# Performance work log

Hardware: AMD Instinct MI355X
Metric: run time of the kernel (lower is better)

Reference implementation:

```python
import jax, jax.numpy as jnp
import numpy as np

N = 50000       # nodes
E = 800000      # edges (avg degree 16)
H2, H1, D_IN = 64, 128, 256
BN_EPS = 1e-5


def setup_inputs() -> dict:
    key = jax.random.key(0)
    ks = jax.random.split(key, 8)
    return {
        "y_features": jax.random.normal(ks[0], (N, H2), dtype=jnp.float32),
        "edge_src": jax.random.randint(ks[1], (E,), 0, N, dtype=jnp.int32),
        "edge_dst": jax.random.randint(ks[2], (E,), 0, N, dtype=jnp.int32),
        "edge_weight": jax.random.uniform(ks[3], (E,), dtype=jnp.float32),
        "W1": jax.random.normal(ks[4], (H2, H1), dtype=jnp.float32) * (1.0 / np.sqrt(H2)),
        "gamma1": jnp.ones((H1,), jnp.float32),
        "beta1": jnp.zeros((H1,), jnp.float32),
        "W2": jax.random.normal(ks[5], (H1, D_IN), dtype=jnp.float32) * (1.0 / np.sqrt(H1)),
        "gamma2": jnp.ones((D_IN,), jnp.float32),
        "beta2": jnp.zeros((D_IN,), jnp.float32),
    }


def _gcn_layer(x, W, src, dst, w):
    # dropout(p=0) -> support = x @ W -> spmm(adj, support) -> ReLU
    support = x @ W                                   # [N, Dout]
    msgs = support[src] * w[:, None]                  # [E, Dout]
    agg = jax.ops.segment_sum(msgs, dst, num_segments=N)
    return jax.nn.relu(agg)


def _batchnorm(h, gamma, beta):
    # BatchNorm1d in training mode: batch stats over nodes, biased variance
    mean = jnp.mean(h, axis=0)
    var = jnp.var(h, axis=0)
    return gamma * (h - mean) * jax.lax.rsqrt(var + BN_EPS) + beta


def reference(y_features, edge_src, edge_dst, edge_weight,
              W1, gamma1, beta1, W2, gamma2, beta2):
    h1 = _gcn_layer(y_features, W1, edge_src, edge_dst, edge_weight)
    h1 = _batchnorm(h1, gamma1, beta1)
    h2 = _gcn_layer(h1, W2, edge_src, edge_dst, edge_weight)
    h2 = _batchnorm(h2, gamma2, beta2)
    return h2
```

## Files before the change

### kernel.cpp

```cpp
#include <hip/hip_runtime.h>

#define NN 50000
#define NE 800000

typedef unsigned short ushort_t;
typedef __attribute__((ext_vector_type(8))) short short8;
typedef __attribute__((ext_vector_type(4))) float f32x4;

constexpr int NB   = (NN + 127) / 128;
constexpr int BCAP = 4096;
constexpr int CH     = 1024;
constexpr int NBLK_E = (NE + CH - 1) / CH;
constexpr int NBLK_M = (NN + 63) / 64;
constexpr int NY4    = NN * 64 / 4;
constexpr int CVT_N  = NY4 + 128 * 64 + 256 * 128 + 768;

__device__ __forceinline__ float bf2f(ushort_t u) {
    union { unsigned int i; float f; } v;
    v.i = ((unsigned int)u) << 16;
    return v.f;
}
__device__ __forceinline__ float bf2f_u(unsigned int lo16) {
    union { unsigned int i; float f; } v;
    v.i = lo16 << 16;
    return v.f;
}
__device__ __forceinline__ float hi16_as_f(unsigned int u) {
    union { unsigned int i; float f; } v;
    v.i = u & 0xffff0000u;
    return v.f;
}
__device__ __forceinline__ ushort_t f2bf(float f) {
    union { float f; unsigned int u; } v;
    v.f = f;
    unsigned int r = (v.u + 0x7fffu + ((v.u >> 16) & 1u)) >> 16;
    return (ushort_t)r;
}


__global__ void cvt_all_k(const float* __restrict__ y, const float* __restrict__ W1,
                          const float* __restrict__ W2, ushort_t* __restrict__ ybf,
                          ushort_t* __restrict__ w1t, ushort_t* __restrict__ w2t,
                          float* __restrict__ stats) {
    int i = blockIdx.x * blockDim.x + threadIdx.x;
    if (i < NY4) {
        float4 v = reinterpret_cast<const float4*>(y)[i];
        ushort4 o;
        o.x = f2bf(v.x); o.y = f2bf(v.y); o.z = f2bf(v.z); o.w = f2bf(v.w);
        reinterpret_cast<ushort4*>(ybf)[i] = o;
    } else if (i < NY4 + 128 * 64) {
        int j = i - NY4;
        int c = j >> 6, k = j & 63;
        w1t[j] = f2bf(W1[k * 128 + c]);
    } else if (i < NY4 + 128 * 64 + 256 * 128) {
        int j = i - NY4 - 128 * 64;
        int c = j >> 7, k = j & 127;
        w2t[j] = f2bf(W2[k * 256 + c]);
    } else if (i < CVT_N) {
        stats[i - (NY4 + 128 * 64 + 256 * 128)] = 0.f;
    }
}


__global__ void bblk_k(const int* __restrict__ src, const int* __restrict__ dst,
                       const float* __restrict__ w, uint2* __restrict__ tmp,
                       int* __restrict__ cnt, int E) {
    __shared__ int lcnt[NB], lcur[NB];
    __shared__ int sm[256];
    __shared__ uint2 rec[CH];
    int b = blockIdx.x, tid = threadIdx.x;
    int e0 = b * CH;
    int ec = min(CH, E - e0);
    for (int i = tid; i < NB; i += 256) lcnt[i] = 0;
    __syncthreads();
    for (int i = tid; i < ec; i += 256)
        atomicAdd(&lcnt[dst[e0 + i] >> 7], 1);
    __syncthreads();
    {
        int i0 = tid * 2;
        int v0 = (i0 < NB) ? lcnt[i0] : 0;
        int v1 = (i0 + 1 < NB) ? lcnt[i0 + 1] : 0;
        int s = v0 + v1;
        sm[tid] = s;
        __syncthreads();
        for (int off = 1; off < 256; off <<= 1) {
            int x = (tid >= off) ? sm[tid - off] : 0;
            __syncthreads();
            sm[tid] += x;
            __syncthreads();
        }
        int excl = sm[tid] - s;
        if (i0 < NB) lcur[i0] = excl;
        if (i0 + 1 < NB) lcur[i0 + 1] = excl + v0;
    }
    __syncthreads();
    for (int q = tid; q < NB; q += 256)
        cnt[q * NBLK_E + b] = (lcnt[q] << 16) | lcur[q];
    __syncthreads();
    for (int i = tid; i < ec; i += 256) {
        int d = dst[e0 + i];
        int p = atomicAdd(&lcur[d >> 7], 1);
        uint2 r;
        r.x = (unsigned int)src[e0 + i] | ((unsigned int)(d & 127) << 16);
        r.y = ((unsigned int)f2bf(w[e0 + i])) << 16;
        rec[p] = r;
    }
    __syncthreads();
    for (int i = tid; i < ec; i += 256)
        tmp[(size_t)e0 + i] = rec[i];
}

__global__ void bstat_k(const int* __restrict__ cnt, int* __restrict__ btot) {
    __shared__ int red[256];
    int q = blockIdx.x, tid = threadIdx.x;
    int s = 0;
    for (int b = tid; b < NBLK_E; b += 256) s += cnt[q * NBLK_E + b] >> 16;
    red[tid] = s;
    __syncthreads();
    for (int off = 128; off > 0; off >>= 1) {
        if (tid < off) red[tid] += red[tid + off];
        __syncthreads();
    }
    if (tid == 0) btot[q] = red[0];
}

__global__ void bsort_k(const uint2* __restrict__ tmp, const int* __restrict__ cnt,
                        const int* __restrict__ btot, int* __restrict__ rp,
                        unsigned int* __restrict__ epack, int n) {
    __shared__ int rstart[NBLK_E + 1], rlofs[NBLK_E], rcnt[NBLK_E];
    __shared__ int c128[128], cur128[128], ex128[128];
    __shared__ int pre[256];
    __shared__ int s_start;
    __shared__ uint2 rec8[BCAP];
    __shared__ unsigned int spk[BCAP];
    int q = blockIdx.x, tid = threadIdx.x;
    int d0 = q * 128;
    for (int b = tid; b < NBLK_E; b += 256) {
        int v = cnt[q * NBLK_E + b];
        rcnt[b]  = v >> 16;
        rlofs[b] = v & 0xffff;
    }
    if (tid < 128) c128[tid] = 0;
    {
        int part = 0;
        for (int b = tid; b < q; b += 256) part += btot[b];
        pre[tid] = part;
        __syncthreads();
        for (int off = 128; off > 0; off >>= 1) {
            if (tid < off) pre[tid] += pre[tid + off];
            __syncthreads();
        }
        if (tid == 0) {
            s_start = pre[0];
            if (q == 0) rp[n] = NE;
        }
        __syncthreads();
    }
    int start = s_start;
    {
        int b0 = tid * 4;
        int w0 = (b0 + 0 < NBLK_E) ? rcnt[b0 + 0] : 0;
        int w1 = (b0 + 1 < NBLK_E) ? rcnt[b0 + 1] : 0;
        int w2 = (b0 + 2 < NBLK_E) ? rcnt[b0 + 2] : 0;
        int w3 = (b0 + 3 < NBLK_E) ? rcnt[b0 + 3] : 0;
        int s = w0 + w1 + w2 + w3;
        pre[tid] = s;
        __syncthreads();
        for (int off = 1; off < 256; off <<= 1) {
            int x = (tid >= off) ? pre[tid - off] : 0;
            __syncthreads();
            pre[tid] += x;
            __syncthreads();
        }
        int excl = pre[tid] - s;
        if (b0 + 0 < NBLK_E) rstart[b0 + 0] = excl;
        if (b0 + 1 < NBLK_E) rstart[b0 + 1] = excl + w0;
        if (b0 + 2 < NBLK_E) rstart[b0 + 2] = excl + w0 + w1;
        if (b0 + 3 < NBLK_E) rstart[b0 + 3] = excl + w0 + w1 + w2;
        if (tid == 255) rstart[NBLK_E] = pre[255];
    }
    __syncthreads();
    int total = min(rstart[NBLK_E], BCAP);
    for (int i = tid; i < total; i += 256) {
        int lo = 0, hi = NBLK_E;
        while (hi - lo > 1) {
            int mid = (lo + hi) >> 1;
            if (rstart[mid] <= i) lo = mid; else hi = mid;
        }
        uint2 r = tmp[(size_t)lo * CH + rlofs[lo] + (i - rstart[lo])];
        rec8[i] = r;
        atomicAdd(&c128[(r.x >> 16) & 127], 1);
    }
    __syncthreads();
    if (tid == 0) {
        int run = 0;
        for (int d = 0; d < 128; ++d) { ex128[d] = run; cur128[d] = run; run += c128[d]; }
    }
    __syncthreads();
    if (tid < 128 && d0 + tid < n) rp[d0 + tid] = start + ex128[tid];
    for (int i = tid; i < total; i += 256) {
        uint2 r = rec8[i];
        int p = atomicAdd(&cur128[(r.x >> 16) & 127], 1);
        spk[p] = r.y | (r.x & 0xffffu);
    }
    __syncthreads();
    for (int i = tid; i < total; i += 256)
        epack[start + i] = spk[i];
}


__global__ void spmm1_k(const ushort_t* __restrict__ yb, const int* __restrict__ rp,
                        const unsigned int* __restrict__ ep,
                        ushort_t* __restrict__ t1, int n) {
    int wid  = (blockIdx.x * blockDim.x + threadIdx.x) >> 6;
    int lane = threadIdx.x & 63;
    if (wid >= n) return;
    int beg = rp[wid], end = rp[wid + 1];
    float acc = 0.f;
    int p = beg;
    for (; p + 16 <= end; p += 16) {
        unsigned int m[16];
#pragma unroll
        for (int j = 0; j < 16; ++j) m[j] = ep[p + j];
        ushort_t u[16];
#pragma unroll
        for (int j = 0; j < 16; ++j)
            u[j] = yb[(size_t)(m[j] & 0xffffu) * 64 + lane];
#pragma unroll
        for (int j = 0; j < 16; ++j)
            acc = fmaf(hi16_as_f(m[j]), bf2f(u[j]), acc);
    }
    for (; p + 4 <= end; p += 4) {
        unsigned int m[4];
#pragma unroll
        for (int j = 0; j < 4; ++j) m[j] = ep[p + j];
        ushort_t u[4];
#pragma unroll
        for (int j = 0; j < 4; ++j)
            u[j] = yb[(size_t)(m[j] & 0xffffu) * 64 + lane];
#pragma unroll
        for (int j = 0; j < 4; ++j)
            acc = fmaf(hi16_as_f(m[j]), bf2f(u[j]), acc);
    }
    for (; p < end; ++p) {
        unsigned int m = ep[p];
        acc = fmaf(hi16_as_f(m), bf2f(yb[(size_t)(m & 0xffffu) * 64 + lane]), acc);
    }
    t1[(size_t)wid * 64 + lane] = f2bf(acc);
}

__global__ void spmm2_k(const ushort_t* __restrict__ h1, const int* __restrict__ rp,
                        const unsigned int* __restrict__ ep,
                        const float* __restrict__ colsum1, const float* __restrict__ colsq1,
                        const float* __restrict__ gamma1, const float* __restrict__ beta1,
                        ushort_t* __restrict__ a2, int n) {
    int wid  = (blockIdx.x * blockDim.x + threadIdx.x) >> 6;
    int lane = threadIdx.x & 63;
    if (wid >= n) return;
    int beg = rp[wid], end = rp[wid + 1];
    float a0 = 0.f, a1 = 0.f, wacc = 0.f;
    int p = beg;
    for (; p + 16 <= end; p += 16) {
        unsigned int m[16];
#pragma unroll
        for (int j = 0; j < 16; ++j) m[j] = ep[p + j];
        unsigned int u[16];
#pragma unroll
        for (int j = 0; j < 16; ++j)
            u[j] = *reinterpret_cast<const unsigned int*>(
                h1 + (size_t)(m[j] & 0xffffu) * 128 + lane * 2);
#pragma unroll
        for (int j = 0; j < 16; ++j) {
            float wt = hi16_as_f(m[j]);
            wacc += wt;
            a0 = fmaf(wt, bf2f_u(u[j] & 0xffffu), a0);
            a1 = fmaf(wt, bf2f_u(u[j] >> 16), a1);
        }
    }
    for (; p + 4 <= end; p += 4) {
        unsigned int m[4];
#pragma unroll
        for (int j = 0; j < 4; ++j) m[j] = ep[p + j];
        unsigned int u[4];
#pragma unroll
        for (int j = 0; j < 4; ++j)
            u[j] = *reinterpret_cast<const unsigned int*>(
                h1 + (size_t)(m[j] & 0xffffu) * 128 + lane * 2);
#pragma unroll
        for (int j = 0; j < 4; ++j) {
            float wt = hi16_as_f(m[j]);
            wacc += wt;
            a0 = fmaf(wt, bf2f_u(u[j] & 0xffffu), a0);
            a1 = fmaf(wt, bf2f_u(u[j] >> 16), a1);
        }
    }
    for (; p < end; ++p) {
        unsigned int m = ep[p];
        float wt = hi16_as_f(m);
        wacc += wt;
        unsigned int u = *reinterpret_cast<const unsigned int*>(
            h1 + (size_t)(m & 0xffffu) * 128 + lane * 2);
        a0 = fmaf(wt, bf2f_u(u & 0xffffu), a0);
        a1 = fmaf(wt, bf2f_u(u >> 16), a1);
    }
    float2 cs = *reinterpret_cast<const float2*>(colsum1 + lane * 2);
    float2 cq = *reinterpret_cast<const float2*>(colsq1 + lane * 2);
    float2 g  = *reinterpret_cast<const float2*>(gamma1 + lane * 2);
    float2 be = *reinterpret_cast<const float2*>(beta1 + lane * 2);
    float m0 = cs.x * (1.0f / NN);
    float v0 = cq.x * (1.0f / NN) - m0 * m0;
    float sc0 = g.x * rsqrtf(v0 + 1e-5f);
    float bi0 = be.x - m0 * sc0;
    float m1 = cs.y * (1.0f / NN);
    float v1 = cq.y * (1.0f / NN) - m1 * m1;
    float sc1 = g.y * rsqrtf(v1 + 1e-5f);
    float bi1 = be.y - m1 * sc1;
    unsigned int o = (unsigned int)f2bf(fmaf(a0, sc0, wacc * bi0))
                   | ((unsigned int)f2bf(fmaf(a1, sc1, wacc * bi1)) << 16);
    *reinterpret_cast<unsigned int*>(a2 + (size_t)wid * 128 + lane * 2) = o;
}


template <int K>
__launch_bounds__(256, 4)
__global__ void mgemm_k(const ushort_t* __restrict__ A, const ushort_t* __restrict__ BT,
                        ushort_t* __restrict__ Cout, float* __restrict__ psum,
                        float* __restrict__ psq, int n, int N) {
    constexpr int K2 = K * 2;
    __shared__ char As[64 * K2];
    __shared__ float lsum[128], lsq[128];
    int tid = threadIdx.x;
    int r0  = blockIdx.x * 64;
    int c0  = blockIdx.y * 128;

    if (tid < 128) { lsum[tid] = 0.f; lsq[tid] = 0.f; }

    {
        const char* Ab = (const char*)(A + (size_t)r0 * K);
#pragma unroll
        for (int it = 0; it < (64 * K2) / 4096; ++it) {
            int p   = (it * 256 + tid) * 16;
            int row = p / K2;
            int cb  = p - row * K2;
            short8 v = *reinterpret_cast<const short8*>(Ab + p);
            *reinterpret_cast<short8*>(As + row * K2 + (cb ^ ((row & 7) << 4))) = v;
        }
    }

    int lane = tid & 63;
    int w    = tid >> 6;
    int wm0  = (w >> 1) * 32;
    int wn0  = (w & 1) * 64;
    int kg   = lane >> 4;
    int lr   = lane & 15;

    short8 bfrag[K / 32][4];
#pragma unroll
    for (int fn = 0; fn < 4; ++fn) {
        const ushort_t* bp = BT + (size_t)(c0 + wn0 + fn * 16 + lr) * K + kg * 8;
#pragma unroll
        for (int ks = 0; ks < K / 32; ++ks)
            bfrag[ks][fn] = *reinterpret_cast<const short8*>(bp + ks * 32);
    }

    __syncthreads();

    f32x4 acc[2][4];
#pragma unroll
    for (int i = 0; i < 2; ++i)
#pragma unroll
        for (int j = 0; j < 4; ++j) acc[i][j] = f32x4{0.f, 0.f, 0.f, 0.f};

#pragma unroll
    for (int ks = 0; ks < K / 32; ++ks) {
        int boff = ks * 64 + kg * 16;
        int row0 = wm0 + lr;
        int row1 = wm0 + 16 + lr;
        short8 a0 = *reinterpret_cast<const short8*>(As + row0 * K2 + (boff ^ ((row0 & 7) << 4)));
        short8 a1 = *reinterpret_cast<const short8*>(As + row1 * K2 + (boff ^ ((row1 & 7) << 4)));
#pragma unroll
        for (int fn = 0; fn < 4; ++fn) {
            acc[0][fn] = __builtin_amdgcn_mfma_f32_16x16x32_bf16(a0, bfrag[ks][fn], acc[0][fn], 0, 0, 0);
            acc[1][fn] = __builtin_amdgcn_mfma_f32_16x16x32_bf16(a1, bfrag[ks][fn], acc[1][fn], 0, 0, 0);
        }
    }

    float s_c[4] = {0.f, 0.f, 0.f, 0.f};
    float q_c[4] = {0.f, 0.f, 0.f, 0.f};
#pragma unroll
    for (int fm = 0; fm < 2; ++fm) {
        int rowb = r0 + wm0 + fm * 16 + kg * 4;
#pragma unroll
        for (int i = 0; i < 4; ++i) {
            int r = rowb + i;
            if (r < n) {
#pragma unroll
                for (int fn = 0; fn < 4; ++fn) {
                    float v = fmaxf(acc[fm][fn][i], 0.f);
                    s_c[fn] += v;
                    q_c[fn] += v * v;
                    int c = c0 + wn0 + fn * 16 + lr;
                    Cout[(size_t)r * N + c] = f2bf(v);
                }
            }
        }
    }
#pragma unroll
    for (int fn = 0; fn < 4; ++fn) {
        float s = s_c[fn], q = q_c[fn];
        s += __shfl_xor(s, 16); q += __shfl_xor(q, 16);
        s += __shfl_xor(s, 32); q += __shfl_xor(q, 32);
        if (lane < 16) {
            int c = wn0 + fn * 16 + lane;
            atomicAdd(&lsum[c], s);
            atomicAdd(&lsq[c], q);
        }
    }
    __syncthreads();
    if (tid < 128) {
        psum[(size_t)blockIdx.x * N + c0 + tid] = lsum[tid];
        psq [(size_t)blockIdx.x * N + c0 + tid] = lsq[tid];
    }
}


template <int F>
__global__ void red_k(const float* __restrict__ psum, const float* __restrict__ psq,
                      float* __restrict__ colsum, float* __restrict__ colsq, int nblk) {
    constexpr int RG = 256 / F;
    __shared__ float ls[256], lq[256];
    int tid = threadIdx.x;
    int c   = tid & (F - 1);
    int rg  = tid / F;
    float s = 0.f, q = 0.f;
    for (int b = blockIdx.x * RG + rg; b < nblk; b += gridDim.x * RG) {
        s += psum[(size_t)b * F + c];
        q += psq [(size_t)b * F + c];
    }
    ls[tid] = s; lq[tid] = q;
    __syncthreads();
    if (tid < F) {
#pragma unroll
        for (int g = 1; g < RG; ++g) { s += ls[g * F + tid]; q += lq[g * F + tid]; }
        atomicAdd(&colsum[tid], s);
        atomicAdd(&colsq[tid], q);
    }
}

__global__ void norm_out_k(const ushort_t* __restrict__ h2, float* __restrict__ out,
                           const float* __restrict__ colsum2, const float* __restrict__ colsq2,
                           const float* __restrict__ gamma2, const float* __restrict__ beta2,
                           int n8) {
    int i = blockIdx.x * blockDim.x + threadIdx.x;
    int stride = gridDim.x * blockDim.x;
    int c = (i * 8) & 255;
    float4 s0, s1, b0, b1;
    {
        float sc[8], bi[8];
#pragma unroll
        for (int j = 0; j < 8; ++j) {
            float m = colsum2[c + j] * (1.0f / NN);
            float v = colsq2[c + j] * (1.0f / NN) - m * m;
            float s = gamma2[c + j] * rsqrtf(v + 1e-5f);
            sc[j] = s;
            bi[j] = beta2[c + j] - m * s;
        }
        s0 = float4{sc[0], sc[1], sc[2], sc[3]};
        s1 = float4{sc[4], sc[5], sc[6], sc[7]};
        b0 = float4{bi[0], bi[1], bi[2], bi[3]};
        b1 = float4{bi[4], bi[5], bi[6], bi[7]};
    }
    for (; i < n8; i += stride) {
        short8 v = reinterpret_cast<const short8*>(h2)[i];
        float4 o0, o1;
        o0.x = fmaf(bf2f((ushort_t)v[0]), s0.x, b0.x);
        o0.y = fmaf(bf2f((ushort_t)v[1]), s0.y, b0.y);
        o0.z = fmaf(bf2f((ushort_t)v[2]), s0.z, b0.z);
        o0.w = fmaf(bf2f((ushort_t)v[3]), s0.w, b0.w);
        o1.x = fmaf(bf2f((ushort_t)v[4]), s1.x, b1.x);
        o1.y = fmaf(bf2f((ushort_t)v[5]), s1.y, b1.y);
        o1.z = fmaf(bf2f((ushort_t)v[6]), s1.z, b1.z);
        o1.w = fmaf(bf2f((ushort_t)v[7]), s1.w, b1.w);
        reinterpret_cast<float4*>(out)[i * 2 + 0] = o0;
        reinterpret_cast<float4*>(out)[i * 2 + 1] = o1;
    }
}


extern "C" void kernel_launch(void* const* d_in, const int* in_sizes, int n_in,
                              void* d_out, int out_size, void* d_ws, size_t ws_size,
                              hipStream_t stream) {
    const float* y      = (const float*)d_in[0];
    const int*   esrc   = (const int*)d_in[1];
    const int*   edst   = (const int*)d_in[2];
    const float* ew     = (const float*)d_in[3];
    const float* W1     = (const float*)d_in[4];
    const float* gamma1 = (const float*)d_in[5];
    const float* beta1  = (const float*)d_in[6];
    const float* W2     = (const float*)d_in[7];
    const float* gamma2 = (const float*)d_in[8];
    const float* beta2  = (const float*)d_in[9];
    float* out = (float*)d_out;

    char* ws = (char*)d_ws;
    size_t off = 0;
    auto alloc = [&](size_t bytes) -> void* {
        void* p = (void*)(ws + off);
        off += (bytes + 255) & ~(size_t)255;
        return p;
    };
    ushort_t* ybf  = (ushort_t*)alloc((size_t)NN * 64 * 2);
    ushort_t* t1   = (ushort_t*)alloc((size_t)NN * 64 * 2);
    ushort_t* h1   = (ushort_t*)alloc((size_t)NN * 128 * 2);
    ushort_t* a2   = (ushort_t*)alloc((size_t)NN * 128 * 2);
    ushort_t* h2   = (ushort_t*)alloc((size_t)NN * 256 * 2);
    ushort_t* w1t  = (ushort_t*)alloc(128 * 64 * 2);
    ushort_t* w2t  = (ushort_t*)alloc(256 * 128 * 2);
    int*   rp      = (int*)alloc((NN + 1) * 4);
    unsigned int* epack = (unsigned int*)alloc((size_t)NE * 4);
    uint2* tmp8    = (uint2*)alloc((size_t)NE * 8);
    int*   cnt     = (int*)alloc((size_t)NB * NBLK_E * 4);
    int*   btot    = (int*)alloc(NB * 4);
    float* psum1   = (float*)alloc((size_t)NBLK_M * 128 * 4);
    float* psq1    = (float*)alloc((size_t)NBLK_M * 128 * 4);
    float* psum2   = (float*)alloc((size_t)NBLK_M * 256 * 4);
    float* psq2    = (float*)alloc((size_t)NBLK_M * 256 * 4);
    float* stats   = (float*)alloc(768 * 4);
    float* colsum1 = stats;
    float* colsq1  = stats + 128;
    float* colsum2 = stats + 256;
    float* colsq2  = stats + 512;
    (void)alloc(64 * 1024);

    cvt_all_k<<<(CVT_N + 255) / 256, 256, 0, stream>>>(y, W1, W2, ybf, w1t, w2t, stats);

    bblk_k<<<NBLK_E, 256, 0, stream>>>(esrc, edst, ew, tmp8, cnt, NE);
    bstat_k<<<NB, 256, 0, stream>>>(cnt, btot);
    bsort_k<<<NB, 256, 0, stream>>>(tmp8, cnt, btot, rp, epack, NN);

    spmm1_k<<<(NN + 3) / 4, 256, 0, stream>>>(ybf, rp, epack, t1, NN);
    mgemm_k<64><<<dim3(NBLK_M, 1), 256, 0, stream>>>(
        t1, w1t, h1, psum1, psq1, NN, 128);
    red_k<128><<<64, 256, 0, stream>>>(psum1, psq1, colsum1, colsq1, NBLK_M);

    spmm2_k<<<(NN + 3) / 4, 256, 0, stream>>>(h1, rp, epack, colsum1, colsq1,
                                              gamma1, beta1, a2, NN);
    mgemm_k<128><<<dim3(NBLK_M, 2), 256, 0, stream>>>(
        a2, w2t, h2, psum2, psq2, NN, 256);
    red_k<256><<<64, 256, 0, stream>>>(psum2, psq2, colsum2, colsq2, NBLK_M);

    norm_out_k<<<2048, 256, 0, stream>>>(h2, out, colsum2, colsq2, gamma2, beta2,
                                         NN * 256 / 8);
}
```

Before: 154.3 us.

## Merge conversion into edge bucketing kernel and simplify bucket sort gather

The bf16 conversion kernel and the edge block-bucketing kernel are folded into one launch, with block ranges selecting which job each block does, so one launch is saved and the two independent jobs can overlap. The bucket sort kernel drops its per-row prefix scan, its binary search and its shared staging buffer. Instead each thread walks the contiguous run of one source block and reads tmp twice, once for counting and once for scattering. This cuts shared memory and scan work but adds a second global read, and load balance becomes uneven because threads own runs of different lengths.

```diff
diff --git a/kernel.cpp b/kernel.cpp
--- a/kernel.cpp
+++ b/kernel.cpp
@@ -14,6 +14,7 @@
 constexpr int NBLK_M = (NN + 63) / 64;
 constexpr int NY4    = NN * 64 / 4;
 constexpr int CVT_N  = NY4 + 128 * 64 + 256 * 128 + 768;
+constexpr int NBLK_CVT = (CVT_N + 255) / 256;
 
 __device__ __forceinline__ float bf2f(ushort_t u) {
     union { unsigned int i; float f; } v;
@@ -38,76 +39,77 @@
 }
 
 
-__global__ void cvt_all_k(const float* __restrict__ y, const float* __restrict__ W1,
-                          const float* __restrict__ W2, ushort_t* __restrict__ ybf,
-                          ushort_t* __restrict__ w1t, ushort_t* __restrict__ w2t,
-                          float* __restrict__ stats) {
-    int i = blockIdx.x * blockDim.x + threadIdx.x;
-    if (i < NY4) {
-        float4 v = reinterpret_cast<const float4*>(y)[i];
-        ushort4 o;
-        o.x = f2bf(v.x); o.y = f2bf(v.y); o.z = f2bf(v.z); o.w = f2bf(v.w);
-        reinterpret_cast<ushort4*>(ybf)[i] = o;
-    } else if (i < NY4 + 128 * 64) {
-        int j = i - NY4;
-        int c = j >> 6, k = j & 63;
-        w1t[j] = f2bf(W1[k * 128 + c]);
-    } else if (i < NY4 + 128 * 64 + 256 * 128) {
-        int j = i - NY4 - 128 * 64;
-        int c = j >> 7, k = j & 127;
-        w2t[j] = f2bf(W2[k * 256 + c]);
-    } else if (i < CVT_N) {
-        stats[i - (NY4 + 128 * 64 + 256 * 128)] = 0.f;
-    }
-}
-
-
-__global__ void bblk_k(const int* __restrict__ src, const int* __restrict__ dst,
-                       const float* __restrict__ w, uint2* __restrict__ tmp,
-                       int* __restrict__ cnt, int E) {
+__global__ void pre_k(const float* __restrict__ y, const float* __restrict__ W1,
+                      const float* __restrict__ W2, ushort_t* __restrict__ ybf,
+                      ushort_t* __restrict__ w1t, ushort_t* __restrict__ w2t,
+                      float* __restrict__ stats,
+                      const int* __restrict__ src, const int* __restrict__ dst,
+                      const float* __restrict__ w, uint2* __restrict__ tmp,
+                      int* __restrict__ cnt, int E) {
     __shared__ int lcnt[NB], lcur[NB];
     __shared__ int sm[256];
     __shared__ uint2 rec[CH];
-    int b = blockIdx.x, tid = threadIdx.x;
-    int e0 = b * CH;
-    int ec = min(CH, E - e0);
-    for (int i = tid; i < NB; i += 256) lcnt[i] = 0;
-    __syncthreads();
-    for (int i = tid; i < ec; i += 256)
-        atomicAdd(&lcnt[dst[e0 + i] >> 7], 1);
-    __syncthreads();
-    {
-        int i0 = tid * 2;
-        int v0 = (i0 < NB) ? lcnt[i0] : 0;
-        int v1 = (i0 + 1 < NB) ? lcnt[i0 + 1] : 0;
-        int s = v0 + v1;
-        sm[tid] = s;
-        __syncthreads();
-        for (int off = 1; off < 256; off <<= 1) {
-            int x = (tid >= off) ? sm[tid - off] : 0;
+    int tid = threadIdx.x;
+    if (blockIdx.x < NBLK_E) {
+        int b = blockIdx.x;
+        int e0 = b * CH;
+        int ec = min(CH, E - e0);
+        for (int i = tid; i < NB; i += 256) lcnt[i] = 0;
+        __syncthreads();
+        for (int i = tid; i < ec; i += 256)
+            atomicAdd(&lcnt[dst[e0 + i] >> 7], 1);
+        __syncthreads();
+        {
+            int i0 = tid * 2;
+            int v0 = (i0 < NB) ? lcnt[i0] : 0;
+            int v1 = (i0 + 1 < NB) ? lcnt[i0 + 1] : 0;
+            int s = v0 + v1;
+            sm[tid] = s;
             __syncthreads();
-            sm[tid] += x;
-            __syncthreads();
-        }
-        int excl = sm[tid] - s;
-        if (i0 < NB) lcur[i0] = excl;
-        if (i0 + 1 < NB) lcur[i0 + 1] = excl + v0;
-    }
-    __syncthreads();
-    for (int q = tid; q < NB; q += 256)
-        cnt[q * NBLK_E + b] = (lcnt[q] << 16) | lcur[q];
-    __syncthreads();
-    for (int i = tid; i < ec; i += 256) {
-        int d = dst[e0 + i];
-        int p = atomicAdd(&lcur[d >> 7], 1);
-        uint2 r;
-        r.x = (unsigned int)src[e0 + i] | ((unsigned int)(d & 127) << 16);
-        r.y = ((unsigned int)f2bf(w[e0 + i])) << 16;
-        rec[p] = r;
-    }
-    __syncthreads();
-    for (int i = tid; i < ec; i += 256)
-        tmp[(size_t)e0 + i] = rec[i];
+            for (int off = 1; off < 256; off <<= 1) {
+                int x = (tid >= off) ? sm[tid - off] : 0;
+                __syncthreads();
+                sm[tid] += x;
+                __syncthreads();
+            }
+            int excl = sm[tid] - s;
+            if (i0 < NB) lcur[i0] = excl;
+            if (i0 + 1 < NB) lcur[i0 + 1] = excl + v0;
+        }
+        __syncthreads();
+        for (int q = tid; q < NB; q += 256)
+            cnt[q * NBLK_E + b] = (lcnt[q] << 16) | lcur[q];
+        __syncthreads();
+        for (int i = tid; i < ec; i += 256) {
+            int d = dst[e0 + i];
+            int p = atomicAdd(&lcur[d >> 7], 1);
+            uint2 r;
+            r.x = (unsigned int)src[e0 + i] | ((unsigned int)(d & 127) << 16);
+            r.y = ((unsigned int)f2bf(w[e0 + i])) << 16;
+            rec[p] = r;
+        }
+        __syncthreads();
+        for (int i = tid; i < ec; i += 256)
+            tmp[(size_t)e0 + i] = rec[i];
+    } else {
+        int i = (blockIdx.x - NBLK_E) * 256 + tid;
+        if (i < NY4) {
+            float4 v = reinterpret_cast<const float4*>(y)[i];
+            ushort4 o;
+            o.x = f2bf(v.x); o.y = f2bf(v.y); o.z = f2bf(v.z); o.w = f2bf(v.w);
+            reinterpret_cast<ushort4*>(ybf)[i] = o;
+        } else if (i < NY4 + 128 * 64) {
+            int j = i - NY4;
+            int c = j >> 6, k = j & 63;
+            w1t[j] = f2bf(W1[k * 128 + c]);
+        } else if (i < NY4 + 128 * 64 + 256 * 128) {
+            int j = i - NY4 - 128 * 64;
+            int c = j >> 7, k = j & 127;
+            w2t[j] = f2bf(W2[k * 256 + c]);
+        } else if (i < CVT_N) {
+            stats[i - (NY4 + 128 * 64 + 256 * 128)] = 0.f;
+        }
+    }
 }
 
 __global__ void bstat_k(const int* __restrict__ cnt, int* __restrict__ btot) {
@@ -127,19 +129,14 @@
 __global__ void bsort_k(const uint2* __restrict__ tmp, const int* __restrict__ cnt,
                         const int* __restrict__ btot, int* __restrict__ rp,
                         unsigned int* __restrict__ epack, int n) {
-    __shared__ int rstart[NBLK_E + 1], rlofs[NBLK_E], rcnt[NBLK_E];
+    __shared__ int cntrow[NBLK_E];
     __shared__ int c128[128], cur128[128], ex128[128];
     __shared__ int pre[256];
     __shared__ int s_start;
-    __shared__ uint2 rec8[BCAP];
     __shared__ unsigned int spk[BCAP];
     int q = blockIdx.x, tid = threadIdx.x;
     int d0 = q * 128;
-    for (int b = tid; b < NBLK_E; b += 256) {
-        int v = cnt[q * NBLK_E + b];
-        rcnt[b]  = v >> 16;
-        rlofs[b] = v & 0xffff;
-    }
+    for (int b = tid; b < NBLK_E; b += 256) cntrow[b] = cnt[q * NBLK_E + b];
     if (tid < 128) c128[tid] = 0;
     {
         int part = 0;
@@ -157,39 +154,13 @@
         __syncthreads();
     }
     int start = s_start;
-    {
-        int b0 = tid * 4;
-        int w0 = (b0 + 0 < NBLK_E) ? rcnt[b0 + 0] : 0;
-        int w1 = (b0 + 1 < NBLK_E) ? rcnt[b0 + 1] : 0;
-        int w2 = (b0 + 2 < NBLK_E) ? rcnt[b0 + 2] : 0;
-        int w3 = (b0 + 3 < NBLK_E) ? rcnt[b0 + 3] : 0;
-        int s = w0 + w1 + w2 + w3;
-        pre[tid] = s;
-        __syncthreads();
-        for (int off = 1; off < 256; off <<= 1) {
-            int x = (tid >= off) ? pre[tid - off] : 0;
-            __syncthreads();
-            pre[tid] += x;
-            __syncthreads();
-        }
-        int excl = pre[tid] - s;
-        if (b0 + 0 < NBLK_E) rstart[b0 + 0] = excl;
-        if (b0 + 1 < NBLK_E) rstart[b0 + 1] = excl + w0;
-        if (b0 + 2 < NBLK_E) rstart[b0 + 2] = excl + w0 + w1;
-        if (b0 + 3 < NBLK_E) rstart[b0 + 3] = excl + w0 + w1 + w2;
-        if (tid == 255) rstart[NBLK_E] = pre[255];
-    }
-    __syncthreads();
-    int total = min(rstart[NBLK_E], BCAP);
-    for (int i = tid; i < total; i += 256) {
-        int lo = 0, hi = NBLK_E;
-        while (hi - lo > 1) {
-            int mid = (lo + hi) >> 1;
-            if (rstart[mid] <= i) lo = mid; else hi = mid;
-        }
-        uint2 r = tmp[(size_t)lo * CH + rlofs[lo] + (i - rstart[lo])];
-        rec8[i] = r;
-        atomicAdd(&c128[(r.x >> 16) & 127], 1);
+    int total = min(btot[q], BCAP);
+    for (int b = tid; b < NBLK_E; b += 256) {
+        int v = cntrow[b];
+        int cN = v >> 16, lo = v & 0xffff;
+        const uint2* tp = tmp + (size_t)b * CH + lo;
+        for (int k = 0; k < cN; ++k)
+            atomicAdd(&c128[(tp[k].x >> 16) & 127], 1);
     }
     __syncthreads();
     if (tid == 0) {
@@ -198,10 +169,15 @@
     }
     __syncthreads();
     if (tid < 128 && d0 + tid < n) rp[d0 + tid] = start + ex128[tid];
-    for (int i = tid; i < total; i += 256) {
-        uint2 r = rec8[i];
-        int p = atomicAdd(&cur128[(r.x >> 16) & 127], 1);
-        spk[p] = r.y | (r.x & 0xffffu);
+    for (int b = tid; b < NBLK_E; b += 256) {
+        int v = cntrow[b];
+        int cN = v >> 16, lo = v & 0xffff;
+        const uint2* tp = tmp + (size_t)b * CH + lo;
+        for (int k = 0; k < cN; ++k) {
+            uint2 r = tp[k];
+            int p = atomicAdd(&cur128[(r.x >> 16) & 127], 1);
+            if (p < BCAP) spk[p] = r.y | (r.x & 0xffffu);
+        }
     }
     __syncthreads();
     for (int i = tid; i < total; i += 256)
@@ -532,9 +508,9 @@
     float* colsq2  = stats + 512;
     (void)alloc(64 * 1024);
 
-    cvt_all_k<<<(CVT_N + 255) / 256, 256, 0, stream>>>(y, W1, W2, ybf, w1t, w2t, stats);
-
-    bblk_k<<<NBLK_E, 256, 0, stream>>>(esrc, edst, ew, tmp8, cnt, NE);
+    pre_k<<<NBLK_E + NBLK_CVT, 256, 0, stream>>>(
+        y, W1, W2, ybf, w1t, w2t, stats, esrc, edst, ew, tmp8, cnt, NE);
+
     bstat_k<<<NB, 256, 0, stream>>>(cnt, btot);
     bsort_k<<<NB, 256, 0, stream>>>(tmp8, cnt, btot, rp, epack, NN);
 
```

Measured after the change: 162.7 us. +5.4%, slower.
